# Performance work log

Measured on AMD Instinct MI355X. Metric: run time of the kernel, lower is better.

The kernel has to match this reference:

```python
import jax, jax.numpy as jnp
import numpy as np

B, S, E, H, V = 32, 256, 300, 256, 100000
NUM_TAGS = 17
T = NUM_TAGS + 2          # +START/STOP (NCRF++ style)
START, STOP = T - 2, T - 1


def setup_inputs() -> dict:
    key = jax.random.key(0)
    ks = jax.random.split(key, 12)
    word_input = jax.random.randint(ks[0], (B, S), 0, V)
    lengths = jax.random.randint(ks[1], (B,), S // 2, S + 1)
    input_mask = (jnp.arange(S)[None, :] < lengths[:, None]).astype(jnp.int32)
    labels = jax.random.randint(ks[2], (B, S), 0, NUM_TAGS)
    labels_token = jax.random.randint(ks[3], (B, S), 0, 2)
    sc = 0.08
    word_emb = jax.random.normal(ks[4], (V, E), dtype=jnp.float32) * sc
    Wih_f = jax.random.normal(ks[5], (4 * H, E), dtype=jnp.float32) * sc
    Whh_f = jax.random.normal(ks[6], (4 * H, H), dtype=jnp.float32) * sc
    Wih_b = jax.random.normal(ks[7], (4 * H, E), dtype=jnp.float32) * sc
    Whh_b = jax.random.normal(ks[8], (4 * H, H), dtype=jnp.float32) * sc
    bih_f = jnp.zeros((4 * H,), jnp.float32)
    bhh_f = jnp.zeros((4 * H,), jnp.float32)
    bih_b = jnp.zeros((4 * H,), jnp.float32)
    bhh_b = jnp.zeros((4 * H,), jnp.float32)
    W_tag = jax.random.normal(ks[9], (T, 2 * H), dtype=jnp.float32) * sc
    b_tag = jnp.zeros((T,), jnp.float32)
    trans = jax.random.normal(ks[10], (T, T), dtype=jnp.float32) * 0.01
    return dict(word_input=word_input, input_mask=input_mask, labels=labels,
                labels_token=labels_token, data_type=1, word_emb=word_emb,
                Wih_f=Wih_f, Whh_f=Whh_f, bih_f=bih_f, bhh_f=bhh_f,
                Wih_b=Wih_b, Whh_b=Whh_b, bih_b=bih_b, bhh_b=bhh_b,
                W_tag=W_tag, b_tag=b_tag, trans=trans)


def _lstm_dir(x, Wih, Whh, bih, bhh, reverse):
    # x: [B,S,E] -> h: [B,S,H]; PyTorch gate order i,f,g,o
    Hd = Whh.shape[1]
    def step(carry, xt):
        h, c = carry
        g = xt @ Wih.T + bih + h @ Whh.T + bhh
        i, f, gg, o = jnp.split(g, 4, axis=-1)
        c = jax.nn.sigmoid(f) * c + jax.nn.sigmoid(i) * jnp.tanh(gg)
        h = jax.nn.sigmoid(o) * jnp.tanh(c)
        return (h, c), h
    h0 = jnp.zeros((x.shape[0], Hd), x.dtype)
    _, hs = jax.lax.scan(step, (h0, h0), x.transpose(1, 0, 2), reverse=reverse)
    return hs.transpose(1, 0, 2)


def _crf_nll(emit, mask, labels, trans):
    # emit: [B,S,T], mask: [B,S] int, labels: [B,S]. Returns summed NLL over batch.
    mf = mask.astype(emit.dtype)
    b = emit.shape[0]
    # gold path score
    prev = jnp.concatenate([jnp.full((b, 1), START, labels.dtype), labels[:, :-1]], axis=1)
    trans_sc = trans[prev, labels]
    emit_sc = jnp.take_along_axis(emit, labels[..., None], axis=-1)[..., 0]
    gold = jnp.sum((trans_sc + emit_sc) * mf, axis=1)
    lengths = mask.sum(axis=1).astype(jnp.int32)
    last_tag = jnp.take_along_axis(labels, (lengths - 1)[:, None], axis=1)[:, 0]
    gold = gold + trans[last_tag, STOP]
    # log partition (forward algorithm)
    alpha0 = emit[:, 0] + trans[START][None, :]
    def step(alpha, inp):
        e_t, m_t = inp  # [B,T], [B]
        new = jax.nn.logsumexp(alpha[:, :, None] + trans[None], axis=1) + e_t
        return jnp.where(m_t[:, None] > 0, new, alpha), None
    alpha, _ = jax.lax.scan(step, alpha0,
                            (emit[:, 1:].transpose(1, 0, 2), mask[:, 1:].transpose(1, 0)))
    logZ = jax.nn.logsumexp(alpha + trans[:, STOP][None, :], axis=1)
    return jnp.sum(logZ - gold)


def _viterbi(emit, mask, trans):
    b, s, t = emit.shape
    delta0 = emit[:, 0] + trans[START][None, :]
    idT = jnp.arange(t)[None, :]
    def step(delta, inp):
        e_t, m_t = inp
        cand = delta[:, :, None] + trans[None]       # [B, prev, cur]
        best_prev = jnp.argmax(cand, axis=1)          # [B,T]
        new = jnp.max(cand, axis=1) + e_t
        delta = jnp.where(m_t[:, None] > 0, new, delta)
        ptr = jnp.where(m_t[:, None] > 0, best_prev, idT)  # identity pass-through when padded
        return delta, ptr
    delta, ptrs = jax.lax.scan(step, delta0,
                               (emit[:, 1:].transpose(1, 0, 2), mask[:, 1:].transpose(1, 0)))
    final = delta + trans[:, STOP][None, :]
    best_last = jnp.argmax(final, axis=1)             # [B]
    score = jnp.max(final, axis=1)
    bidx = jnp.arange(b)
    def back(tag, ptr_t):
        return ptr_t[bidx, tag], tag
    tag0, ys = jax.lax.scan(back, best_last, ptrs, reverse=True)  # ys[i]=tag at time i+1
    tags = jnp.concatenate([tag0[:, None], ys.transpose(1, 0)], axis=1)  # [B,S]
    tags = tags * mask.astype(tags.dtype)
    return score, tags


def reference(word_input, input_mask, labels, labels_token, data_type, word_emb,
              Wih_f, Whh_f, bih_f, bhh_f, Wih_b, Whh_b, bih_b, bhh_b,
              W_tag, b_tag, trans):
    # data_type==1 -> cyber branch (Python int, resolved at trace time)
    x = word_emb[word_input] * input_mask[..., None].astype(word_emb.dtype)
    hf = _lstm_dir(x, Wih_f, Whh_f, bih_f, bhh_f, reverse=False)
    hb = _lstm_dir(x, Wih_b, Whh_b, bih_b, bhh_b, reverse=True)
    out = jnp.concatenate([hf, hb], axis=-1)          # [B,S,2H]; dropout = identity (eval)
    logits = out @ W_tag.T + b_tag                    # [B,S,T]
    crf_loss = _crf_nll(logits, input_mask, labels, trans)
    ans_loss = crf_loss / word_input.shape[0]
    _, tag_seq = _viterbi(logits, input_mask, trans)
    return ans_loss, tag_seq
```

## Files before the change

kernel.cpp:

```cpp
#include <hip/hip_runtime.h>
#include <hip/hip_fp16.h>
#include <math.h>

#define BB 32
#define SS 256
#define EE 300
#define KP 320
#define HH 256
#define TT 19
#define START_TAG 17
#define STOP_TAG 18
#define BS 8192
#define GIN_PER_DIR (8192*1024)

#define RCH 12
#define LDS_WCHUNK (16 - RCH)
#define K_LSTM_LDS_BYTES ((8192 + 32 + 256) * 16)

#define EMBED_BLKS 1280
#define W16N_BLKS  329
#define WHH_BLKS   1024

typedef _Float16 half8 __attribute__((ext_vector_type(8)));
typedef float    f32x4 __attribute__((ext_vector_type(4)));

__device__ __forceinline__ float fexp(float x){
#if defined(__has_builtin) && __has_builtin(__builtin_amdgcn_exp2f)
  return __builtin_amdgcn_exp2f(x * 1.4426950408889634f);
#else
  return expf(x);
#endif
}
__device__ __forceinline__ float frcp(float x){
#if defined(__has_builtin) && __has_builtin(__builtin_amdgcn_rcpf)
  return __builtin_amdgcn_rcpf(x);
#else
  return 1.0f/x;
#endif
}
__device__ __forceinline__ float sigm(float x){ return frcp(1.0f + fexp(-x)); }
__device__ __forceinline__ float ftanh(float x){
  x = fminf(fmaxf(x, -20.f), 20.f);
  float e = fexp(2.0f*x);
  return (e - 1.0f) * frcp(e + 1.0f);
}

#ifdef __has_builtin
#if __has_builtin(__builtin_amdgcn_fdot2)
#define HAVE_FDOT2 1
#endif
#endif

__device__ __forceinline__ float dot2(unsigned int w, unsigned int h, float acc){
#ifdef HAVE_FDOT2
  typedef _Float16 h2_t __attribute__((ext_vector_type(2)));
  return __builtin_amdgcn_fdot2(__builtin_bit_cast(h2_t, w),
                                __builtin_bit_cast(h2_t, h), acc, false);
#else
  float r;
  asm("v_dot2_f32_f16 %0, %1, %2, %3" : "=v"(r) : "v"(w), "v"(h), "v"(acc));
  return r;
#endif
}

__device__ __forceinline__ uint4 vload_u4(const uint4* p){
  uint4 r;
  asm volatile("global_load_dwordx4 %0, %1, off"
               : "=&v"(r) : "v"(p) : "memory");
  return r;
}

__device__ __forceinline__ unsigned int pack_h2(float a, float b){
  unsigned int lo = __half_as_ushort(__float2half(a));
  unsigned int hi = __half_as_ushort(__float2half(b));
  return (hi << 16) | lo;
}

__device__ __forceinline__ void mac4(uint4 w0, uint4 w1, uint4 w2, uint4 w3, uint4 hu,
                                     float& ai, float& af, float& ag, float& ao){
  ai = dot2(w0.x, hu.x, ai); ai = dot2(w0.y, hu.y, ai); ai = dot2(w0.z, hu.z, ai); ai = dot2(w0.w, hu.w, ai);
  af = dot2(w1.x, hu.x, af); af = dot2(w1.y, hu.y, af); af = dot2(w1.z, hu.z, af); af = dot2(w1.w, hu.w, af);
  ag = dot2(w2.x, hu.x, ag); ag = dot2(w2.y, hu.y, ag); ag = dot2(w2.z, hu.z, ag); ag = dot2(w2.w, hu.w, ag);
  ao = dot2(w3.x, hu.x, ao); ao = dot2(w3.y, hu.y, ao); ao = dot2(w3.z, hu.z, ao); ao = dot2(w3.w, hu.w, ao);
}


__global__ void k_prep(const int* __restrict__ wi, const int* __restrict__ msk,
                       const float* __restrict__ emb,
                       const float* __restrict__ Wih_f, const float* __restrict__ Wih_b,
                       const float* __restrict__ bih_f, const float* __restrict__ bhh_f,
                       const float* __restrict__ bih_b, const float* __restrict__ bhh_b,
                       const float* __restrict__ Whh_f, const float* __restrict__ Whh_b,
                       unsigned int* __restrict__ x16, unsigned int* __restrict__ w16n,
                       float* __restrict__ bias, unsigned int* __restrict__ whh16){
  unsigned bx = blockIdx.x;
  if (bx < EMBED_BLKS){
    int id = bx*256 + threadIdx.x;
    if (id >= BS*40) return;
    int row = id / 40, q = id - row*40;
    int base = wi[row]*300;
    float m = (float)msk[row];
    float v[8];
    #pragma unroll
    for (int e = 0; e < 8; ++e){
      int k = q*8 + e;
      v[e] = (k < 300) ? emb[base + k]*m : 0.f;
    }
    uint4 o;
    o.x = pack_h2(v[0], v[1]); o.y = pack_h2(v[2], v[3]);
    o.z = pack_h2(v[4], v[5]); o.w = pack_h2(v[6], v[7]);
    ((uint4*)x16)[id] = o;
  } else if (bx < EMBED_BLKS + W16N_BLKS){
    int id = (bx - EMBED_BLKS)*256 + threadIdx.x;
    if (id < 2048*40){
      int n = id / 40, q = id - n*40;
      int dd = n >> 10, r = n & 1023, j = r >> 2, g = r & 3;
      const float* W = dd ? Wih_b : Wih_f;
      int base = (g*256 + j)*300;
      float v[8];
      #pragma unroll
      for (int e = 0; e < 8; ++e){
        int k = q*8 + e;
        v[e] = (k < 300) ? W[base + k] : 0.f;
      }
      uint4 o;
      o.x = pack_h2(v[0], v[1]); o.y = pack_h2(v[2], v[3]);
      o.z = pack_h2(v[4], v[5]); o.w = pack_h2(v[6], v[7]);
      ((uint4*)w16n)[id] = o;
    } else {
      int n = id - 2048*40;
      if (n < 2048){
        int dd = n >> 10, r = n & 1023, j = r >> 2, g = r & 3;
        int orow = g*256 + j;
        bias[n] = dd ? (bih_b[orow] + bhh_b[orow]) : (bih_f[orow] + bhh_f[orow]);
      }
    }
  } else {
    int id = (bx - EMBED_BLKS - W16N_BLKS)*256 + threadIdx.x;
    int j   = id & 3;
    int u4  = id >> 2;
    int tid = u4 & 511;
    int q   = (u4 >> 9) & 63;
    int d   = u4 >> 15;
    int kpart = tid >> 8, urow = tid & 255;
    int u = q >> 2, g = q & 3;
    int k = kpart*128 + u*8 + j*2;
    const float* W = d ? Whh_b : Whh_f;
    float w0 = W[(size_t)(g*256 + urow)*256 + k];
    float w1 = W[(size_t)(g*256 + urow)*256 + k + 1];
    whh16[id] = pack_h2(w0, w1);
  }
}

__global__ __launch_bounds__(256) void k_gemm(const unsigned short* __restrict__ x16,
      const unsigned short* __restrict__ w16n, const float* __restrict__ bias,
      float* __restrict__ gin){
  int tid = threadIdx.x;
  int l = tid & 63, w = tid >> 6;
  int lm = l & 15, kg = l >> 4;
  int m0 = blockIdx.y * 64;
  int nw = blockIdx.x * 64 + w*16;
  const uint4* A  = ((const uint4*)x16) + (size_t)(m0 + lm)*40 + kg;
  const uint4* Bp = ((const uint4*)w16n) + (size_t)(nw + lm)*40 + kg;
  f32x4 acc0 = {0.f,0.f,0.f,0.f}, acc1 = acc0, acc2 = acc0, acc3 = acc0;
  #pragma unroll
  for (int kt = 0; kt < 10; ++kt){
    half8 b  = __builtin_bit_cast(half8, Bp[kt*4]);
    half8 a0 = __builtin_bit_cast(half8, A[       kt*4]);
    half8 a1 = __builtin_bit_cast(half8, A[ 640 + kt*4]);
    half8 a2 = __builtin_bit_cast(half8, A[1280 + kt*4]);
    half8 a3 = __builtin_bit_cast(half8, A[1920 + kt*4]);
    acc0 = __builtin_amdgcn_mfma_f32_16x16x32_f16(a0, b, acc0, 0, 0, 0);
    acc1 = __builtin_amdgcn_mfma_f32_16x16x32_f16(a1, b, acc1, 0, 0, 0);
    acc2 = __builtin_amdgcn_mfma_f32_16x16x32_f16(a2, b, acc2, 0, 0, 0);
    acc3 = __builtin_amdgcn_mfma_f32_16x16x32_f16(a3, b, acc3, 0, 0, 0);
  }
  int n = nw + lm;
  float bn = bias[n];
  int dd = n >> 10, r = n & 1023;
  float* go = gin + (size_t)dd*GIN_PER_DIR + r;
  int mb = m0 + kg*4;
  #pragma unroll
  for (int reg = 0; reg < 4; ++reg){
    go[(size_t)(mb +  0 + reg)*1024] = acc0[reg] + bn;
    go[(size_t)(mb + 16 + reg)*1024] = acc1[reg] + bn;
    go[(size_t)(mb + 32 + reg)*1024] = acc2[reg] + bn;
    go[(size_t)(mb + 48 + reg)*1024] = acc3[reg] + bn;
  }
}

__global__ __launch_bounds__(512, 2) void k_lstm(const float* __restrict__ gin,
                 const uint4* __restrict__ W16, float* __restrict__ hseq){
  extern __shared__ uint4 smem[];
  uint4*  wlds = smem;
  uint4*  hsq  = smem + 8192;
  float4* glh  = (float4*)(smem + 8224);

  int tid = threadIdx.x;
  int b = blockIdx.x & 31, d = blockIdx.x >> 5;
  int kpart = tid >> 8;
  const uint4* wq = W16 + (size_t)d*64*512 + tid;
  const float* gb = gin + (size_t)d*GIN_PER_DIR + (size_t)b*SS*1024;

  #pragma unroll
  for (int q = 4*RCH; q < 64; ++q)
    wlds[(q - 4*RCH)*512 + tid] = wq[(size_t)q*512];

  if (tid < 32) hsq[tid] = make_uint4(0u,0u,0u,0u);

  uint4 wr[4*RCH];
  #pragma unroll
  for (int q = 0; q < 4*RCH; ++q) wr[q] = vload_u4(wq + (size_t)q*512);
  asm volatile("s_waitcnt vmcnt(0)" ::: "memory");
  __builtin_amdgcn_sched_barrier(0);

  float c = 0.f;
  __syncthreads();

  const uint4* wl = wlds + tid;
  for (int s = 0; s < SS; ++s){
    int t = d ? (SS-1-s) : s;
    float4 gv = make_float4(0.f,0.f,0.f,0.f);
    if (tid < 256) gv = ((const float4*)(gb + (size_t)t*1024))[tid];

    float ai = 0.f, af = 0.f, ag = 0.f, ao = 0.f;
    #pragma unroll
    for (int u = 0; u < RCH; ++u){
      uint4 hu = hsq[kpart*16 + u];
      mac4(wr[u*4+0], wr[u*4+1], wr[u*4+2], wr[u*4+3], hu, ai, af, ag, ao);
    }
    #pragma unroll
    for (int uu = 0; uu < LDS_WCHUNK; ++uu){
      uint4 hu = hsq[kpart*16 + RCH + uu];
      uint4 w0 = wl[(uu*4+0)*512];
      uint4 w1 = wl[(uu*4+1)*512];
      uint4 w2 = wl[(uu*4+2)*512];
      uint4 w3 = wl[(uu*4+3)*512];
      mac4(w0, w1, w2, w3, hu, ai, af, ag, ao);
    }
    if (kpart) glh[tid & 255] = make_float4(ai, af, ag, ao);
    __syncthreads();
    if (tid < 256){
      float4 p1 = glh[tid];
      float iv = sigm (ai + p1.x + gv.x);
      float fv = sigm (af + p1.y + gv.y);
      float gg = ftanh(ag + p1.z + gv.z);
      float ov = sigm (ao + p1.w + gv.w);
      c = fv*c + iv*gg;
      float hv = ov*ftanh(c);
      hseq[((size_t)(b*SS + t))*512 + d*256 + tid] = hv;
      float hp = __shfl_xor(hv, 1);
      if (!(tid & 1))
        ((unsigned int*)hsq)[tid >> 1] = pack_h2(hv, hp);
    }
    __syncthreads();
  }
}

__global__ void k_emit(const float* __restrict__ hseq, const float* __restrict__ Wtag,
                       const float* __restrict__ btag, float* __restrict__ emit){
  int id = blockIdx.x*256 + threadIdx.x;
  if (id >= BS*TT) return;
  int row = id / TT, tg = id - row*TT;
  const float4* hp = (const float4*)(hseq + (size_t)row*512);
  const float4* wp = (const float4*)(Wtag + (size_t)tg*512);
  float acc = btag[tg];
  #pragma unroll 8
  for (int k = 0; k < 128; ++k){
    float4 h = hp[k], w = wp[k];
    acc += h.x*w.x + h.y*w.y + h.z*w.z + h.w*w.w;
  }
  emit[id] = acc;
}

__global__ __launch_bounds__(64) void k_crfvit(const float* __restrict__ emit,
                         const int* __restrict__ msk,
                         const int* __restrict__ lab, const float* __restrict__ trans,
                         float* __restrict__ nll, float* __restrict__ out){
  int tid = threadIdx.x;
  __shared__ float tr[361];
  __shared__ float eb[SS*TT];
  __shared__ int   ml[SS];
  __shared__ int   ll[SS];
  __shared__ unsigned short pv[SS*TT];
  __shared__ float al[TT];
  __shared__ int   tg[SS];

  int b = blockIdx.x & 31;
  const float* ebg = emit + (size_t)b*SS*TT;
  for (int i = tid; i < 361; i += 64) tr[i] = trans[i];
  for (int i = tid; i < SS*TT; i += 64) eb[i] = ebg[i];
  for (int i = tid; i < SS; i += 64) ml[i] = msk[b*SS + i];

  if (blockIdx.x < 32){
    for (int i = tid; i < SS; i += 64) ll[i] = lab[b*SS + i];
    __syncthreads();
    float gp = 0.f; int ln = 0;
    for (int t = tid; t < SS; t += 64){
      int m = ml[t];
      ln += m;
      if (m){
        int l = ll[t];
        int p = t ? ll[t-1] : START_TAG;
        gp += tr[p*19 + l] + eb[t*19 + l];
      }
    }
    for (int off = 32; off; off >>= 1){ gp += __shfl_down(gp, off); ln += __shfl_down(ln, off); }
    float gold = 0.f;
    if (tid == 0){
      int lt = ll[ln - 1];
      gold = gp + tr[lt*19 + STOP_TAG];
    }
    if (tid < 19) al[tid] = eb[tid] + tr[START_TAG*19 + tid];
    __syncthreads();
    for (int t = 1; t < SS; ++t){
      float nv = 0.f;
      if (tid < 19){
        float mx = -1e30f;
        #pragma unroll
        for (int p = 0; p < 19; ++p){ float v = al[p] + tr[p*19 + tid]; mx = fmaxf(mx, v); }
        float sum = 0.f;
        #pragma unroll
        for (int p = 0; p < 19; ++p) sum += fexp(al[p] + tr[p*19 + tid] - mx);
        nv = mx + logf(sum) + eb[t*19 + tid];
      }
      __syncthreads();
      if (tid < 19 && ml[t]) al[tid] = nv;
      __syncthreads();
    }
    if (tid == 0){
      float mx = -1e30f;
      for (int c2 = 0; c2 < 19; ++c2) mx = fmaxf(mx, al[c2] + tr[c2*19 + STOP_TAG]);
      float sum = 0.f;
      for (int c2 = 0; c2 < 19; ++c2) sum += fexp(al[c2] + tr[c2*19 + STOP_TAG] - mx);
      nll[b] = (mx + logf(sum)) - gold;
    }
  } else {
    if (tid < 19) al[tid] = eb[tid] + tr[START_TAG*19 + tid];
    __syncthreads();
    for (int t = 1; t < SS; ++t){
      int m = ml[t];
      float best = -1e30f; int bp = 0;
      if (tid < 19){
        #pragma unroll
        for (int p = 0; p < 19; ++p){
          float v = al[p] + tr[p*19 + tid];
          if (v > best){ best = v; bp = p; }
        }
      }
      __syncthreads();
      if (tid < 19){
        if (m){ al[tid] = best + eb[t*19 + tid]; pv[t*19 + tid] = (unsigned short)bp; }
        else  { pv[t*19 + tid] = (unsigned short)tid; }
      }
      __syncthreads();
    }
    if (tid == 0){
      float bv = -1e30f; int bl = 0;
      for (int c2 = 0; c2 < 19; ++c2){
        float v = al[c2] + tr[c2*19 + STOP_TAG];
        if (v > bv){ bv = v; bl = c2; }
      }
      tg[SS-1] = bl;
      for (int t = SS-1; t > 0; --t) tg[t-1] = pv[t*19 + tg[t]];
    }
    __syncthreads();
    for (int t = tid; t < SS; t += 64)
      out[1 + b*SS + t] = (float)(tg[t] * ml[t]);
  }
}

__global__ void k_final(const float* __restrict__ nll, float* __restrict__ out){
  int tid = threadIdx.x;
  float v = (tid < 32) ? nll[tid] : 0.f;
  for (int off = 32; off; off >>= 1) v += __shfl_down(v, off);
  if (tid == 0) out[0] = v * (1.0f/32.0f);
}

extern "C" void kernel_launch(void* const* d_in, const int* in_sizes, int n_in,
                              void* d_out, int out_size, void* d_ws, size_t ws_size,
                              hipStream_t stream){
  const int*   wi    = (const int*)d_in[0];
  const int*   msk   = (const int*)d_in[1];
  const int*   lab   = (const int*)d_in[2];
  const float* emb   = (const float*)d_in[5];
  const float* Wih_f = (const float*)d_in[6];
  const float* Whh_f = (const float*)d_in[7];
  const float* bih_f = (const float*)d_in[8];
  const float* bhh_f = (const float*)d_in[9];
  const float* Wih_b = (const float*)d_in[10];
  const float* Whh_b = (const float*)d_in[11];
  const float* bih_b = (const float*)d_in[12];
  const float* bhh_b = (const float*)d_in[13];
  const float* Wtag  = (const float*)d_in[14];
  const float* btag  = (const float*)d_in[15];
  const float* trans = (const float*)d_in[16];

  float* ws   = (float*)d_ws;
  unsigned short* x16  = (unsigned short*)ws;
  unsigned short* w16n = (unsigned short*)(ws + 2490368);
  float* bias = ws + 3112960;
  unsigned int* W16u = (unsigned int*)(ws + 3115008);
  uint4* W16  = (uint4*)W16u;
  float* gin  = ws + 3639296;
  float* hseq = ws + 20416512;
  float* emit = ws + 24610816;
  float* nll  = ws + 24922112;
  float* out  = (float*)d_out;

  static bool s_attr = false;
  if (!s_attr){
    (void)hipFuncSetAttribute((const void*)k_lstm,
                              hipFuncAttributeMaxDynamicSharedMemorySize,
                              K_LSTM_LDS_BYTES);
    s_attr = true;
  }

  hipLaunchKernelGGL(k_prep, dim3(EMBED_BLKS + W16N_BLKS + WHH_BLKS), dim3(256), 0, stream,
                     wi, msk, emb, Wih_f, Wih_b, bih_f, bhh_f, bih_b, bhh_b,
                     Whh_f, Whh_b, (unsigned int*)x16, (unsigned int*)w16n, bias, W16u);
  hipLaunchKernelGGL(k_gemm,   dim3(32,128),  dim3(256),  0, stream, x16, w16n, bias, gin);
  hipLaunchKernelGGL(k_lstm,   dim3(64),      dim3(512),  K_LSTM_LDS_BYTES, stream,
                     gin, W16, hseq);
  hipLaunchKernelGGL(k_emit,   dim3(608),     dim3(256),  0, stream, hseq, Wtag, btag, emit);
  hipLaunchKernelGGL(k_crfvit, dim3(64),      dim3(64),   0, stream, emit, msk, lab, trans,
                     nll, out);
  hipLaunchKernelGGL(k_final,  dim3(1),       dim3(64),   0, stream, nll, out);
}
```

Measured before the change: 860.6 us.

## Use K-major staging layouts, LDS-staged coalesced GEMM stores, and LDS tag weights

Prep kernels now write the fp16 embedding and Wih copies in a K-chunk-major layout using float4 loads, so the GEMM's per-lane fragment loads become contiguous across lanes. The GEMM epilogue stages its accumulators through a shared-memory tile and writes float4 rows to gin, replacing strided scalar stores. The emission kernel caches W_tag and b_tag in LDS. The total runtime is probably dominated by the sequential LSTM kernel, which is untouched, so the overall gain is bounded. The extra LDS traffic and one block barrier in the GEMM are small costs.

Measured after the change: 759.0 us. -11.8%, faster.

```diff
diff --git a/kernel.cpp b/kernel.cpp
--- a/kernel.cpp
+++ b/kernel.cpp
@@ -97,35 +97,28 @@
   if (bx < EMBED_BLKS){
     int id = bx*256 + threadIdx.x;
     if (id >= BS*40) return;
-    int row = id / 40, q = id - row*40;
-    int base = wi[row]*300;
+    int q = id >> 13, row = id & 8191;
     float m = (float)msk[row];
-    float v[8];
-    #pragma unroll
-    for (int e = 0; e < 8; ++e){
-      int k = q*8 + e;
-      v[e] = (k < 300) ? emb[base + k]*m : 0.f;
-    }
+    const float4* e4 = (const float4*)emb + (size_t)wi[row]*75 + q*2;
+    float4 v0 = make_float4(0.f,0.f,0.f,0.f), v1 = v0;
+    if (q <= 37) v0 = e4[0];
+    if (q <= 36) v1 = e4[1];
     uint4 o;
-    o.x = pack_h2(v[0], v[1]); o.y = pack_h2(v[2], v[3]);
-    o.z = pack_h2(v[4], v[5]); o.w = pack_h2(v[6], v[7]);
+    o.x = pack_h2(v0.x*m, v0.y*m); o.y = pack_h2(v0.z*m, v0.w*m);
+    o.z = pack_h2(v1.x*m, v1.y*m); o.w = pack_h2(v1.z*m, v1.w*m);
     ((uint4*)x16)[id] = o;
   } else if (bx < EMBED_BLKS + W16N_BLKS){
     int id = (bx - EMBED_BLKS)*256 + threadIdx.x;
     if (id < 2048*40){
-      int n = id / 40, q = id - n*40;
+      int kc = id >> 11, n = id & 2047;
       int dd = n >> 10, r = n & 1023, j = r >> 2, g = r & 3;
-      const float* W = dd ? Wih_b : Wih_f;
-      int base = (g*256 + j)*300;
-      float v[8];
-      #pragma unroll
-      for (int e = 0; e < 8; ++e){
-        int k = q*8 + e;
-        v[e] = (k < 300) ? W[base + k] : 0.f;
-      }
+      const float4* W4 = (const float4*)(dd ? Wih_b : Wih_f) + (size_t)(g*256 + j)*75 + kc*2;
+      float4 v0 = make_float4(0.f,0.f,0.f,0.f), v1 = v0;
+      if (kc <= 37) v0 = W4[0];
+      if (kc <= 36) v1 = W4[1];
       uint4 o;
-      o.x = pack_h2(v[0], v[1]); o.y = pack_h2(v[2], v[3]);
-      o.z = pack_h2(v[4], v[5]); o.w = pack_h2(v[6], v[7]);
+      o.x = pack_h2(v0.x, v0.y); o.y = pack_h2(v0.z, v0.w);
+      o.z = pack_h2(v1.x, v1.y); o.w = pack_h2(v1.z, v1.w);
       ((uint4*)w16n)[id] = o;
     } else {
       int n = id - 2048*40;
@@ -152,40 +145,51 @@
   }
 }
 
-__global__ __launch_bounds__(256) void k_gemm(const unsigned short* __restrict__ x16,
-      const unsigned short* __restrict__ w16n, const float* __restrict__ bias,
+__global__ __launch_bounds__(256) void k_gemm(const uint4* __restrict__ x16k,
+      const uint4* __restrict__ w16k, const float* __restrict__ bias,
       float* __restrict__ gin){
+  __shared__ float Cs[64][68];
   int tid = threadIdx.x;
   int l = tid & 63, w = tid >> 6;
   int lm = l & 15, kg = l >> 4;
   int m0 = blockIdx.y * 64;
-  int nw = blockIdx.x * 64 + w*16;
-  const uint4* A  = ((const uint4*)x16) + (size_t)(m0 + lm)*40 + kg;
-  const uint4* Bp = ((const uint4*)w16n) + (size_t)(nw + lm)*40 + kg;
+  int n0 = blockIdx.x * 64;
+  int nw = n0 + w*16;
+  const uint4* A  = x16k + (size_t)kg*8192 + m0 + lm;
+  const uint4* Bp = w16k + (size_t)kg*2048 + nw + lm;
   f32x4 acc0 = {0.f,0.f,0.f,0.f}, acc1 = acc0, acc2 = acc0, acc3 = acc0;
   #pragma unroll
   for (int kt = 0; kt < 10; ++kt){
-    half8 b  = __builtin_bit_cast(half8, Bp[kt*4]);
-    half8 a0 = __builtin_bit_cast(half8, A[       kt*4]);
-    half8 a1 = __builtin_bit_cast(half8, A[ 640 + kt*4]);
-    half8 a2 = __builtin_bit_cast(half8, A[1280 + kt*4]);
-    half8 a3 = __builtin_bit_cast(half8, A[1920 + kt*4]);
+    half8 b  = __builtin_bit_cast(half8, Bp[(size_t)kt*8192]);
+    half8 a0 = __builtin_bit_cast(half8, A[(size_t)kt*32768      ]);
+    half8 a1 = __builtin_bit_cast(half8, A[(size_t)kt*32768 + 16 ]);
+    half8 a2 = __builtin_bit_cast(half8, A[(size_t)kt*32768 + 32 ]);
+    half8 a3 = __builtin_bit_cast(half8, A[(size_t)kt*32768 + 48 ]);
     acc0 = __builtin_amdgcn_mfma_f32_16x16x32_f16(a0, b, acc0, 0, 0, 0);
     acc1 = __builtin_amdgcn_mfma_f32_16x16x32_f16(a1, b, acc1, 0, 0, 0);
     acc2 = __builtin_amdgcn_mfma_f32_16x16x32_f16(a2, b, acc2, 0, 0, 0);
     acc3 = __builtin_amdgcn_mfma_f32_16x16x32_f16(a3, b, acc3, 0, 0, 0);
   }
-  int n = nw + lm;
-  float bn = bias[n];
-  int dd = n >> 10, r = n & 1023;
-  float* go = gin + (size_t)dd*GIN_PER_DIR + r;
-  int mb = m0 + kg*4;
+  int cl = w*16 + lm;
   #pragma unroll
   for (int reg = 0; reg < 4; ++reg){
-    go[(size_t)(mb +  0 + reg)*1024] = acc0[reg] + bn;
-    go[(size_t)(mb + 16 + reg)*1024] = acc1[reg] + bn;
-    go[(size_t)(mb + 32 + reg)*1024] = acc2[reg] + bn;
-    go[(size_t)(mb + 48 + reg)*1024] = acc3[reg] + bn;
+    Cs[kg*4 + reg     ][cl] = acc0[reg];
+    Cs[kg*4 + reg + 16][cl] = acc1[reg];
+    Cs[kg*4 + reg + 32][cl] = acc2[reg];
+    Cs[kg*4 + reg + 48][cl] = acc3[reg];
+  }
+  __syncthreads();
+  int mloc = tid >> 4, c4 = (tid & 15)*4;
+  int n = n0 + c4;
+  int dd = n >> 10, r = n & 1023;
+  float4 bn = *(const float4*)&bias[n];
+  float* go = gin + (size_t)dd*GIN_PER_DIR + r;
+  #pragma unroll
+  for (int rep = 0; rep < 4; ++rep){
+    int ml = rep*16 + mloc;
+    float4 v = *(const float4*)&Cs[ml][c4];
+    v.x += bn.x; v.y += bn.y; v.z += bn.z; v.w += bn.w;
+    *(float4*)&go[(size_t)(m0 + ml)*1024] = v;
   }
 }
 
@@ -257,17 +261,25 @@
   }
 }
 
-__global__ void k_emit(const float* __restrict__ hseq, const float* __restrict__ Wtag,
+__global__ __launch_bounds__(256) void k_emit(const float* __restrict__ hseq,
+                       const float* __restrict__ Wtag,
                        const float* __restrict__ btag, float* __restrict__ emit){
-  int id = blockIdx.x*256 + threadIdx.x;
+  __shared__ float wt[19][516];
+  __shared__ float bt[19];
+  int tid = threadIdx.x;
+  for (int i = tid; i < 19*512; i += 256) wt[i / 512][i & 511] = Wtag[i];
+  if (tid < 19) bt[tid] = btag[tid];
+  __syncthreads();
+  int id = blockIdx.x*256 + tid;
   if (id >= BS*TT) return;
   int row = id / TT, tg = id - row*TT;
   const float4* hp = (const float4*)(hseq + (size_t)row*512);
-  const float4* wp = (const float4*)(Wtag + (size_t)tg*512);
-  float acc = btag[tg];
+  const float*  wp = &wt[tg][0];
+  float acc = bt[tg];
   #pragma unroll 8
   for (int k = 0; k < 128; ++k){
-    float4 h = hp[k], w = wp[k];
+    float4 h = hp[k];
+    const float4 w = *(const float4*)&wp[k*4];
     acc += h.x*w.x + h.y*w.y + h.z*w.z + h.w*w.w;
   }
   emit[id] = acc;
@@ -419,7 +431,8 @@
   hipLaunchKernelGGL(k_prep, dim3(EMBED_BLKS + W16N_BLKS + WHH_BLKS), dim3(256), 0, stream,
                      wi, msk, emb, Wih_f, Wih_b, bih_f, bhh_f, bih_b, bhh_b,
                      Whh_f, Whh_b, (unsigned int*)x16, (unsigned int*)w16n, bias, W16u);
-  hipLaunchKernelGGL(k_gemm,   dim3(32,128),  dim3(256),  0, stream, x16, w16n, bias, gin);
+  hipLaunchKernelGGL(k_gemm,   dim3(32,128),  dim3(256),  0, stream,
+                     (const uint4*)x16, (const uint4*)w16n, bias, gin);
   hipLaunchKernelGGL(k_lstm,   dim3(64),      dim3(512),  K_LSTM_LDS_BYTES, stream,
                      gin, W16, hseq);
   hipLaunchKernelGGL(k_emit,   dim3(608),     dim3(256),  0, stream, hseq, Wtag, btag, emit);
```
